# Performance work log

Measured on AMD Instinct MI355X. Metric: run time of the kernel, lower is better.

The kernel has to match this reference:

```python
import jax, jax.numpy as jnp
import numpy as np

B = 16384
I = 1024  # inputs_size
H = 1024  # hidden_size


def _linear_params(key, fan_in, fan_out):
    # torch nn.Linear default init: U(-1/sqrt(fan_in), 1/sqrt(fan_in))
    kw, kb = jax.random.split(key)
    bound = 1.0 / np.sqrt(fan_in)
    W = jax.random.uniform(kw, (fan_out, fan_in), jnp.float32, -bound, bound)
    b = jax.random.uniform(kb, (fan_out,), jnp.float32, -bound, bound)
    return W, b


def setup_inputs() -> dict:
    key = jax.random.key(0)
    ks = jax.random.split(key, 8)
    inp = {
        "input": jax.random.normal(ks[0], (B, I), jnp.float32),
        "hidden": jax.random.normal(ks[1], (B, H), jnp.float32),
    }
    names = ["r_i", "r_h", "z_i", "z_h", "n_i", "n_h"]
    fan_ins = [I, H, I, H, I, H]
    for name, fi, k in zip(names, fan_ins, ks[2:]):
        W, b = _linear_params(k, fi, H)
        inp[f"W_{name}"] = W
        inp[f"b_{name}"] = b
    return inp


def reference(input, hidden,
              W_r_i, b_r_i, W_r_h, b_r_h,
              W_z_i, b_z_i, W_z_h, b_z_h,
              W_n_i, b_n_i, W_n_h, b_n_h):
    # Faithful to the original (including its bug: z uses r_layer_h(hidden)).
    r_h = hidden @ W_r_h.T + b_r_h  # reused by both r and z gates
    r = jax.nn.sigmoid(input @ W_r_i.T + b_r_i + r_h)
    z = jax.nn.sigmoid(input @ W_z_i.T + b_z_i + r_h)
    n = jnp.tanh(input @ W_n_i.T + b_n_i + r * (hidden @ W_n_h.T + b_n_h))
    next_hidden = (1.0 - z) * n + z * hidden
    return (next_hidden, next_hidden)
```

## Files before the change

### kernel.cpp

```cpp
#include <hip/hip_runtime.h>


#define BM 128
#define BN 64
#define BK 32

typedef __attribute__((ext_vector_type(8))) short          bf16x8;
typedef __attribute__((ext_vector_type(8))) unsigned short u16x8;
typedef __attribute__((ext_vector_type(4))) float          f32x4;

__device__ __forceinline__ unsigned short f2bf(float f) {
    union { float f; unsigned u; } v; v.f = f;
    unsigned r = v.u + 0x7FFFu + ((v.u >> 16) & 1u);
    return (unsigned short)(r >> 16);
}

__global__ __launch_bounds__(256) void convert_bf16(
    const float* __restrict__ in0, const float* __restrict__ in1,
    const float* __restrict__ w0, const float* __restrict__ w1,
    const float* __restrict__ w2, const float* __restrict__ w3,
    const float* __restrict__ w4, unsigned short* __restrict__ ws)
{
    const long long e = ((long long)blockIdx.x * 256 + threadIdx.x) * 8;
    const float* src;
    if (e < 16777216LL) {
        src = in0 + e;
    } else if (e < 33554432LL) {
        src = in1 + (e - 16777216LL);
    } else {
        const long long t = e - 33554432LL;
        const int g = (int)(t >> 20);
        const long long within = t & 1048575LL;
        const float* w = (g == 0) ? w0 : (g == 1) ? w1 : (g == 2) ? w2 : (g == 3) ? w3 : w4;
        src = w + within;
    }
    const float4 a = *reinterpret_cast<const float4*>(src);
    const float4 b = *reinterpret_cast<const float4*>(src + 4);
    u16x8 o;
    o[0] = f2bf(a.x); o[1] = f2bf(a.y); o[2] = f2bf(a.z); o[3] = f2bf(a.w);
    o[4] = f2bf(b.x); o[5] = f2bf(b.y); o[6] = f2bf(b.z); o[7] = f2bf(b.w);
    *reinterpret_cast<u16x8*>(ws + e) = o;
}

__device__ __forceinline__ void async16(const void* g, void* l) {
    __builtin_amdgcn_global_load_lds(
        (const __attribute__((address_space(1))) unsigned int*)g,
        (__attribute__((address_space(3))) unsigned int*)l, 16, 0, 0);
}

__global__ __launch_bounds__(256, 2) void gru_fused(
    const unsigned short* __restrict__ bf,
    const float* __restrict__ hidden,
    const float* __restrict__ b_ri, const float* __restrict__ b_rh,
    const float* __restrict__ b_zi, const float* __restrict__ b_ni,
    const float* __restrict__ b_nh,
    float* __restrict__ out)
{
    const int H = 1024, K = 1024;
    const int BH = 16384 * 1024;

    __shared__ __align__(16) unsigned char sBuf[36864];

    const int tid  = threadIdx.x;
    const int wave = tid >> 6;
    const int lane = tid & 63;
    const int quad = lane >> 4;
    const int l16  = lane & 15;

    const int row0 = blockIdx.y * BM;
    const int col0 = blockIdx.x * BN;

    const unsigned short* inB  = bf;
    const unsigned short* hidB = bf + 16777216;
    const unsigned short* wB   = bf + 33554432;

    const unsigned short* srcbase[9];
    int ldsoff[9];
    #pragma unroll
    for (int j = 0; j < 9; ++j) {
        const int s = (j * 4 + wave) * 64 + lane;
        ldsoff[j] = s * 16;
        if (s < 512) {
            const int r = s >> 2;
            srcbase[j] = inB + (long long)(row0 + r) * K + (s & 3) * 8;
        } else if (s < 1024) {
            const int r = (s - 512) >> 2;
            srcbase[j] = hidB + (long long)(row0 + r) * K + (s & 3) * 8;
        } else {
            const int t = s - 1024;
            const int g = t >> 8;
            const int tt = t & 255;
            const int n = tt >> 2;
            srcbase[j] = wB + (long long)g * 1048576 + (long long)(col0 + n) * K + (tt & 3) * 8;
        }
    }

    f32x4 acc[5][2][4];
    #pragma unroll
    for (int g = 0; g < 5; ++g)
        #pragma unroll
        for (int mi = 0; mi < 2; ++mi)
            #pragma unroll
            for (int ni = 0; ni < 4; ++ni)
                acc[g][mi][ni] = (f32x4){0.f, 0.f, 0.f, 0.f};

    for (int k0 = 0; k0 < K; k0 += BK) {
        __syncthreads();
        #pragma unroll
        for (int j = 0; j < 9; ++j)
            async16(srcbase[j] + k0, sBuf + ldsoff[j]);
        __syncthreads();

        bf16x8 aIn[2], aHid[2];
        #pragma unroll
        for (int mi = 0; mi < 2; ++mi) {
            const int r = wave * 32 + mi * 16 + l16;
            aIn [mi] = *reinterpret_cast<const bf16x8*>(&sBuf[r * 64 + quad * 16]);
            aHid[mi] = *reinterpret_cast<const bf16x8*>(&sBuf[8192 + r * 64 + quad * 16]);
        }
        #pragma unroll
        for (int g = 0; g < 5; ++g) {
            #pragma unroll
            for (int ni = 0; ni < 4; ++ni) {
                const int n = ni * 16 + l16;
                const bf16x8 b = *reinterpret_cast<const bf16x8*>(
                    &sBuf[16384 + g * 4096 + n * 64 + quad * 16]);
                #pragma unroll
                for (int mi = 0; mi < 2; ++mi) {
                    const bf16x8 a = (g == 1 || g == 4) ? aHid[mi] : aIn[mi];
                    acc[g][mi][ni] = __builtin_amdgcn_mfma_f32_16x16x32_bf16(a, b, acc[g][mi][ni], 0, 0, 0);
                }
            }
        }
    }

    #pragma unroll
    for (int ni = 0; ni < 4; ++ni) {
        const int gcol = col0 + ni * 16 + l16;
        const float bri = b_ri[gcol], brh = b_rh[gcol], bzi = b_zi[gcol];
        const float bni = b_ni[gcol], bnh = b_nh[gcol];
        #pragma unroll
        for (int mi = 0; mi < 2; ++mi) {
            #pragma unroll
            for (int r4 = 0; r4 < 4; ++r4) {
                const int grow = row0 + wave * 32 + mi * 16 + quad * 4 + r4;
                const float g_ri = acc[0][mi][ni][r4];
                const float g_rh = acc[1][mi][ni][r4];
                const float g_zi = acc[2][mi][ni][r4];
                const float g_ni = acc[3][mi][ni][r4];
                const float g_nh = acc[4][mi][ni][r4];
                const float rh = g_rh + brh;
                const float rr = 1.f / (1.f + __expf(-(g_ri + bri + rh)));
                const float zz = 1.f / (1.f + __expf(-(g_zi + bzi + rh)));
                const float nn = tanhf(g_ni + bni + rr * (g_nh + bnh));
                const float h  = hidden[(long long)grow * H + gcol];
                const float o  = (1.f - zz) * nn + zz * h;
                out[(long long)grow * H + gcol]      = o;
                out[BH + (long long)grow * H + gcol] = o;
            }
        }
    }
}

extern "C" void kernel_launch(void* const* d_in, const int* in_sizes, int n_in,
                              void* d_out, int out_size, void* d_ws, size_t ws_size,
                              hipStream_t stream) {
    const float* input  = (const float*)d_in[0];
    const float* hidden = (const float*)d_in[1];
    const float* W_ri = (const float*)d_in[2];
    const float* b_ri = (const float*)d_in[3];
    const float* W_rh = (const float*)d_in[4];
    const float* b_rh = (const float*)d_in[5];
    const float* W_zi = (const float*)d_in[6];
    const float* b_zi = (const float*)d_in[7];
    const float* W_ni = (const float*)d_in[10];
    const float* b_ni = (const float*)d_in[11];
    const float* W_nh = (const float*)d_in[12];
    const float* b_nh = (const float*)d_in[13];
    float* out = (float*)d_out;
    unsigned short* ws = (unsigned short*)d_ws;

    convert_bf16<<<18944, 256, 0, stream>>>(input, hidden, W_ri, W_rh, W_zi, W_ni, W_nh, ws);

    dim3 grid(1024 / BN, 16384 / BM);
    gru_fused<<<grid, 256, 0, stream>>>(ws, hidden, b_ri, b_rh, b_zi, b_ni, b_nh, out);
}
```

Measured before the change: 504.6 us.

## Split waves by input/hidden gates, swizzle LDS, exchange partials via shared memory

Reassigns the work so waves 0-1 compute the three input-side gate GEMMs and waves 2-3 the two hidden-side gates, each over all 128 rows and a 32-column half. An XOR swizzle is applied to the LDS layout to avoid bank conflicts on fragment reads. Hidden-side partial sums are passed to the input waves through shared memory for the epilogue. This cuts redundant A-fragment loads and LDS conflicts, at the cost of uneven per-wave MFMA counts (3 vs 2 gates) and extra syncs and LDS traffic in the epilogue.

```diff
diff --git a/kernel.cpp b/kernel.cpp
--- a/kernel.cpp
+++ b/kernel.cpp
@@ -1,9 +1,5 @@
 #include <hip/hip_runtime.h>
 
-
-#define BM 128
-#define BN 64
-#define BK 32
 
 typedef __attribute__((ext_vector_type(8))) short          bf16x8;
 typedef __attribute__((ext_vector_type(8))) unsigned short u16x8;
@@ -56,9 +52,6 @@
     const float* __restrict__ b_nh,
     float* __restrict__ out)
 {
-    const int H = 1024, K = 1024;
-    const int BH = 16384 * 1024;
-
     __shared__ __align__(16) unsigned char sBuf[36864];
 
     const int tid  = threadIdx.x;
@@ -67,98 +60,151 @@
     const int quad = lane >> 4;
     const int l16  = lane & 15;
 
-    const int row0 = blockIdx.y * BM;
-    const int col0 = blockIdx.x * BN;
-
-    const unsigned short* inB  = bf;
-    const unsigned short* hidB = bf + 16777216;
-    const unsigned short* wB   = bf + 33554432;
-
-    const unsigned short* srcbase[9];
-    int ldsoff[9];
+    const int row0 = blockIdx.y * 128;
+    const int col0 = blockIdx.x * 64;
+
+    const int kchunk = (quad ^ (l16 & 3) ^ ((l16 >> 2) & 3)) & 3;
+
+    int srcoff[9];
     #pragma unroll
     for (int j = 0; j < 9; ++j) {
         const int s = (j * 4 + wave) * 64 + lane;
-        ldsoff[j] = s * 16;
         if (s < 512) {
-            const int r = s >> 2;
-            srcbase[j] = inB + (long long)(row0 + r) * K + (s & 3) * 8;
+            const int r = s >> 2, qh = s & 3;
+            const int p = (qh ^ r ^ (r >> 2)) & 3;
+            srcoff[j] = (row0 + r) * 1024 + p * 8;
         } else if (s < 1024) {
-            const int r = (s - 512) >> 2;
-            srcbase[j] = hidB + (long long)(row0 + r) * K + (s & 3) * 8;
+            const int r = (s - 512) >> 2, qh = s & 3;
+            const int p = (qh ^ r ^ (r >> 2)) & 3;
+            srcoff[j] = 16777216 + (row0 + r) * 1024 + p * 8;
         } else {
             const int t = s - 1024;
-            const int g = t >> 8;
-            const int tt = t & 255;
-            const int n = tt >> 2;
-            srcbase[j] = wB + (long long)g * 1048576 + (long long)(col0 + n) * K + (tt & 3) * 8;
-        }
-    }
-
-    f32x4 acc[5][2][4];
-    #pragma unroll
-    for (int g = 0; g < 5; ++g)
+            const int g = t >> 8, tt = t & 255;
+            const int n = tt >> 2, qh = tt & 3;
+            const int p = (qh ^ n ^ (n >> 2)) & 3;
+            srcoff[j] = 33554432 + g * 1048576 + (col0 + n) * 1024 + p * 8;
+        }
+    }
+    const int ldsbase = wave * 1024 + lane * 16;
+
+    const bool isInput = (wave < 2);
+    const int  nbase   = (wave & 1) * 32;
+
+    const int abase = (isInput ? 0 : 8192) + l16 * 64 + kchunk * 16;
+    const int bb    = 16384 + nbase * 64 + l16 * 64 + kchunk * 16;
+    const int bOff0 = bb + (isInput ? 0 : 1) * 4096;
+    const int bOff1 = bb + (isInput ? 2 : 4) * 4096;
+    const int bOff2 = bb + 3 * 4096;
+
+    f32x4 acc[3][8][2];
+    #pragma unroll
+    for (int g = 0; g < 3; ++g)
         #pragma unroll
-        for (int mi = 0; mi < 2; ++mi)
-            #pragma unroll
-            for (int ni = 0; ni < 4; ++ni)
+        for (int mi = 0; mi < 8; ++mi)
+            #pragma unroll
+            for (int ni = 0; ni < 2; ++ni)
                 acc[g][mi][ni] = (f32x4){0.f, 0.f, 0.f, 0.f};
 
-    for (int k0 = 0; k0 < K; k0 += BK) {
+    for (int k0 = 0; k0 < 1024; k0 += 32) {
         __syncthreads();
         #pragma unroll
         for (int j = 0; j < 9; ++j)
-            async16(srcbase[j] + k0, sBuf + ldsoff[j]);
-        __syncthreads();
-
-        bf16x8 aIn[2], aHid[2];
-        #pragma unroll
-        for (int mi = 0; mi < 2; ++mi) {
-            const int r = wave * 32 + mi * 16 + l16;
-            aIn [mi] = *reinterpret_cast<const bf16x8*>(&sBuf[r * 64 + quad * 16]);
-            aHid[mi] = *reinterpret_cast<const bf16x8*>(&sBuf[8192 + r * 64 + quad * 16]);
-        }
-        #pragma unroll
-        for (int g = 0; g < 5; ++g) {
-            #pragma unroll
-            for (int ni = 0; ni < 4; ++ni) {
-                const int n = ni * 16 + l16;
-                const bf16x8 b = *reinterpret_cast<const bf16x8*>(
-                    &sBuf[16384 + g * 4096 + n * 64 + quad * 16]);
-                #pragma unroll
-                for (int mi = 0; mi < 2; ++mi) {
-                    const bf16x8 a = (g == 1 || g == 4) ? aHid[mi] : aIn[mi];
-                    acc[g][mi][ni] = __builtin_amdgcn_mfma_f32_16x16x32_bf16(a, b, acc[g][mi][ni], 0, 0, 0);
+            async16(bf + srcoff[j] + k0, sBuf + ldsbase + j * 4096);
+        __syncthreads();
+
+        if (isInput) {
+            bf16x8 B[3][2];
+            #pragma unroll
+            for (int ni = 0; ni < 2; ++ni) {
+                B[0][ni] = *reinterpret_cast<const bf16x8*>(&sBuf[bOff0 + ni * 1024]);
+                B[1][ni] = *reinterpret_cast<const bf16x8*>(&sBuf[bOff1 + ni * 1024]);
+                B[2][ni] = *reinterpret_cast<const bf16x8*>(&sBuf[bOff2 + ni * 1024]);
+            }
+            #pragma unroll
+            for (int mi = 0; mi < 8; ++mi) {
+                const bf16x8 A = *reinterpret_cast<const bf16x8*>(&sBuf[abase + mi * 1024]);
+                #pragma unroll
+                for (int g = 0; g < 3; ++g)
+                    #pragma unroll
+                    for (int ni = 0; ni < 2; ++ni)
+                        acc[g][mi][ni] = __builtin_amdgcn_mfma_f32_16x16x32_bf16(A, B[g][ni], acc[g][mi][ni], 0, 0, 0);
+            }
+        } else {
+            bf16x8 B[2][2];
+            #pragma unroll
+            for (int ni = 0; ni < 2; ++ni) {
+                B[0][ni] = *reinterpret_cast<const bf16x8*>(&sBuf[bOff0 + ni * 1024]);
+                B[1][ni] = *reinterpret_cast<const bf16x8*>(&sBuf[bOff1 + ni * 1024]);
+            }
+            #pragma unroll
+            for (int mi = 0; mi < 8; ++mi) {
+                const bf16x8 A = *reinterpret_cast<const bf16x8*>(&sBuf[abase + mi * 1024]);
+                #pragma unroll
+                for (int g = 0; g < 2; ++g)
+                    #pragma unroll
+                    for (int ni = 0; ni < 2; ++ni)
+                        acc[g][mi][ni] = __builtin_amdgcn_mfma_f32_16x16x32_bf16(A, B[g][ni], acc[g][mi][ni], 0, 0, 0);
+            }
+        }
+    }
+
+    float* eBuf = reinterpret_cast<float*>(sBuf);
+
+    float bA[2], bB[2], bC[2];
+    #pragma unroll
+    for (int ni = 0; ni < 2; ++ni) {
+        const int gcol = col0 + nbase + ni * 16 + l16;
+        if (isInput) { bA[ni] = b_ri[gcol]; bB[ni] = b_zi[gcol]; bC[ni] = b_ni[gcol]; }
+        else         { bA[ni] = b_rh[gcol]; bB[ni] = b_nh[gcol]; bC[ni] = 0.f; }
+    }
+
+    __syncthreads();
+
+    #pragma unroll
+    for (int c = 0; c < 2; ++c) {
+        if (!isInput) {
+            #pragma unroll
+            for (int mc = 0; mc < 4; ++mc) {
+                const int mi = c * 4 + mc;
+                #pragma unroll
+                for (int ni = 0; ni < 2; ++ni) {
+                    const int colB = nbase + ni * 16 + l16;
+                    #pragma unroll
+                    for (int r4 = 0; r4 < 4; ++r4) {
+                        const int rowc = mc * 16 + quad * 4 + r4;
+                        eBuf[rowc * 68 + colB]        = acc[0][mi][ni][r4] + bA[ni];
+                        eBuf[4352 + rowc * 68 + colB] = acc[1][mi][ni][r4] + bB[ni];
+                    }
                 }
             }
         }
-    }
-
-    #pragma unroll
-    for (int ni = 0; ni < 4; ++ni) {
-        const int gcol = col0 + ni * 16 + l16;
-        const float bri = b_ri[gcol], brh = b_rh[gcol], bzi = b_zi[gcol];
-        const float bni = b_ni[gcol], bnh = b_nh[gcol];
-        #pragma unroll
-        for (int mi = 0; mi < 2; ++mi) {
-            #pragma unroll
-            for (int r4 = 0; r4 < 4; ++r4) {
-                const int grow = row0 + wave * 32 + mi * 16 + quad * 4 + r4;
-                const float g_ri = acc[0][mi][ni][r4];
-                const float g_rh = acc[1][mi][ni][r4];
-                const float g_zi = acc[2][mi][ni][r4];
-                const float g_ni = acc[3][mi][ni][r4];
-                const float g_nh = acc[4][mi][ni][r4];
-                const float rh = g_rh + brh;
-                const float rr = 1.f / (1.f + __expf(-(g_ri + bri + rh)));
-                const float zz = 1.f / (1.f + __expf(-(g_zi + bzi + rh)));
-                const float nn = tanhf(g_ni + bni + rr * (g_nh + bnh));
-                const float h  = hidden[(long long)grow * H + gcol];
-                const float o  = (1.f - zz) * nn + zz * h;
-                out[(long long)grow * H + gcol]      = o;
-                out[BH + (long long)grow * H + gcol] = o;
-            }
-        }
+        __syncthreads();
+        if (isInput) {
+            #pragma unroll
+            for (int mc = 0; mc < 4; ++mc) {
+                const int mi = c * 4 + mc;
+                #pragma unroll
+                for (int ni = 0; ni < 2; ++ni) {
+                    const int colB = nbase + ni * 16 + l16;
+                    const int gcol = col0 + colB;
+                    #pragma unroll
+                    for (int r4 = 0; r4 < 4; ++r4) {
+                        const int rowc = mc * 16 + quad * 4 + r4;
+                        const int grow = row0 + mi * 16 + quad * 4 + r4;
+                        const float rh = eBuf[rowc * 68 + colB];
+                        const float nh = eBuf[4352 + rowc * 68 + colB];
+                        const float rr = 1.f / (1.f + __expf(-(acc[0][mi][ni][r4] + bA[ni] + rh)));
+                        const float zz = 1.f / (1.f + __expf(-(acc[1][mi][ni][r4] + bB[ni] + rh)));
+                        const float nn = tanhf(acc[2][mi][ni][r4] + bC[ni] + rr * nh);
+                        const float h  = hidden[grow * 1024 + gcol];
+                        const float o  = (1.f - zz) * nn + zz * h;
+                        out[grow * 1024 + gcol]            = o;
+                        out[16777216 + grow * 1024 + gcol] = o;
+                    }
+                }
+            }
+        }
+        __syncthreads();
     }
 }
 
@@ -182,6 +228,6 @@
 
     convert_bf16<<<18944, 256, 0, stream>>>(input, hidden, W_ri, W_rh, W_zi, W_ni, W_nh, ws);
 
-    dim3 grid(1024 / BN, 16384 / BM);
+    dim3 grid(16, 128);
     gru_fused<<<grid, 256, 0, stream>>>(ws, hidden, b_ri, b_rh, b_zi, b_ni, b_nh, out);
 }
```

New measurement: 542.7 us. 7.5% more time.
